# Kernel tuning notes

Hardware: AMD Instinct MI355X
Metric: run time of the kernel (lower is better)

The kernel has to match this reference:

```python
import jax, jax.numpy as jnp
import numpy as np

N_NODES = 50000
N_EDGES = 1600000
N_GRAPHS = 64


def _gcn_conv(x, row, col, ew, W, b, n_nodes):
    # x: [N, Fin] -> [N, Fout]; PyG GCNConv: lin, add self-loops (w=1),
    # symmetric normalization, scatter-add at target (col), + bias.
    x = x @ W
    loop = jnp.arange(n_nodes, dtype=row.dtype)
    r = jnp.concatenate([row, loop])
    c = jnp.concatenate([col, loop])
    w = jnp.concatenate([ew, jnp.ones((n_nodes,), dtype=ew.dtype)])
    deg = jax.ops.segment_sum(w, c, num_segments=n_nodes)
    dinv = jnp.where(deg > 0, jax.lax.rsqrt(jnp.where(deg > 0, deg, 1.0)), 0.0)
    norm = dinv[r] * w * dinv[c]                      # [E+N]
    msg = x[r] * norm[:, None]                        # [E+N, Fout] (dominant traffic)
    out = jax.ops.segment_sum(msg, c, num_segments=n_nodes)
    return out + b


def setup_inputs() -> dict:
    key = jax.random.key(0)
    ks = jax.random.split(key, 12)
    x = jax.random.normal(ks[0], (N_NODES, 128), dtype=jnp.float32)
    edge_index = jax.random.randint(ks[1], (2, N_EDGES), 0, N_NODES, dtype=jnp.int32)
    edge_attr = jax.random.uniform(ks[2], (N_EDGES,), dtype=jnp.float32)
    batch = jnp.sort(jax.random.randint(ks[3], (N_NODES,), 0, N_GRAPHS, dtype=jnp.int32))
    glorot = lambda k, fi, fo: jax.random.normal(k, (fi, fo), jnp.float32) * np.sqrt(2.0 / (fi + fo))
    return {
        "x": x, "edge_index": edge_index, "edge_attr": edge_attr, "batch": batch,
        "W1": glorot(ks[4], 128, 128), "b1": jnp.zeros((128,), jnp.float32),
        "W2": glorot(ks[5], 128, 64), "b2": jnp.zeros((64,), jnp.float32),
        "fc1_W": glorot(ks[6], 64, 128), "fc1_b": jnp.zeros((128,), jnp.float32),
        "fc2_W": glorot(ks[7], 128, 2), "fc2_b": jnp.zeros((2,), jnp.float32),
    }


def reference(x, edge_index, edge_attr, batch, W1, b1, W2, b2, fc1_W, fc1_b, fc2_W, fc2_b):
    row, col = edge_index[0], edge_index[1]
    h = jax.nn.relu(_gcn_conv(x, row, col, edge_attr, W1, b1, N_NODES))
    x1 = jax.nn.relu(_gcn_conv(h, row, col, edge_attr, W2, b2, N_NODES))
    # global mean pool over batch ids
    sums = jax.ops.segment_sum(x1, batch, num_segments=N_GRAPHS)
    cnt = jax.ops.segment_sum(jnp.ones((N_NODES,), x1.dtype), batch, num_segments=N_GRAPHS)
    x2 = sums / jnp.maximum(cnt, 1.0)[:, None]        # [B, 64]
    # dropout is identity in eval mode
    h = jax.nn.relu(x2 @ fc1_W + fc1_b)
    logits = h @ fc2_W + fc2_b                        # [B, 2]
    return jax.nn.log_softmax(logits, axis=1)
```

## Files before the change

kernel.cpp:

```cpp
#include <hip/hip_runtime.h>
#include <hip/hip_bf16.h>


#define CAP 64
#define OVFCAP 8192
#define NRANGE 512
#define MAXNRP 2048
#define BSTR 68
#define KP 136
#define PARTNB 256
#define PBUF 6400

typedef float v2f  __attribute__((ext_vector_type(2)));
typedef float f32x4 __attribute__((ext_vector_type(4)));
typedef short bf16x8 __attribute__((ext_vector_type(8)));

__device__ inline unsigned short f2bf(float f) {
    unsigned u = __float_as_uint(f);
    u += 0x7FFFu + ((u >> 16) & 1u);
    return (unsigned short)(u >> 16);
}
__device__ inline void fp8x4_to_f32(unsigned w, float* o) {
    v2f lo = __builtin_amdgcn_cvt_pk_f32_fp8((int)w, false);
    v2f hi = __builtin_amdgcn_cvt_pk_f32_fp8((int)w, true);
    o[0] = lo[0]; o[1] = lo[1]; o[2] = hi[0]; o[3] = hi[1];
}
__device__ inline unsigned f32x4_to_fp8(float a, float b, float c, float d) {
    int w = 0;
    w = __builtin_amdgcn_cvt_pk_fp8_f32(a, b, w, false);
    w = __builtin_amdgcn_cvt_pk_fp8_f32(c, d, w, true);
    return (unsigned)w;
}
__device__ inline float dinv_of(int ws) {
    return rsqrtf((float)ws * (1.0f / 32768.0f) + 1.0f);
}

__global__ __launch_bounds__(512)
void part_kernel(const int* __restrict__ rows, const int* __restrict__ cols,
                 const float* __restrict__ ew, int* __restrict__ rangeCnt,
                 uint2* __restrict__ rng, int E, int NR, int RSEG,
                 const float* __restrict__ W1, const float* __restrict__ W2,
                 unsigned short* __restrict__ wt1, unsigned short* __restrict__ wt2) {
    const int t = threadIdx.x;
    if (blockIdx.x >= PARTNB) {
        if (blockIdx.x == PARTNB) {
            for (int i = t; i < 128 * 128; i += 512) {
                int c = i >> 7, k = i & 127;
                wt1[c * KP + k] = f2bf(W1[k * 128 + c]);
            }
        } else {
            for (int i = t; i < 64 * 128; i += 512) {
                int c = i >> 7, k = i & 127;
                wt2[c * KP + k] = f2bf(W2[k * 64 + c]);
            }
        }
        return;
    }
    __shared__ uint2 buf[PBUF];
    __shared__ int hcnt[NRANGE];
    __shared__ int lbase[NRANGE];
    __shared__ int gbase[NRANGE];
    __shared__ int wtot[8];
    const int CS = (E + PARTNB - 1) / PARTNB;
    const int e0 = blockIdx.x * CS, e1 = min(e0 + CS, E);
    const int M = e1 - e0;

    if (CS <= PBUF) {
        for (int i = t; i < NRANGE; i += 512) hcnt[i] = 0;
        __syncthreads();
        for (int e = e0 + t; e < e1; e += 512)
            atomicAdd(&hcnt[cols[e] / NR], 1);
        __syncthreads();
        {
            int v = hcnt[t];
            int inc = v;
            #pragma unroll
            for (int off = 1; off < 64; off <<= 1) {
                int n = __shfl_up(inc, off);
                if ((t & 63) >= off) inc += n;
            }
            const int w = t >> 6;
            if ((t & 63) == 63) wtot[w] = inc;
            __syncthreads();
            int wo = 0;
            for (int k = 0; k < w; ++k) wo += wtot[k];
            int excl = wo + inc - v;
            lbase[t] = excl;
            gbase[t] = (v > 0) ? atomicAdd(&rangeCnt[t], v) : 0;
            hcnt[t] = excl;
        }
        __syncthreads();
        for (int e = e0 + t; e < e1; e += 512) {
            int c = cols[e];
            int r = c / NR;
            int q = (int)(ew[e] * 32768.0f);
            if (q > 32767) q = 32767;
            unsigned rec = ((unsigned)rows[e] << 15) | (unsigned)q;
            int p = atomicAdd(&hcnt[r], 1);
            buf[p] = make_uint2((unsigned)c, rec);
        }
        __syncthreads();
        for (int i = t; i < M; i += 512) {
            uint2 u = buf[i];
            int r = (int)u.x / NR;
            int idx = gbase[r] + (i - lbase[r]);
            if (idx < RSEG) rng[(size_t)r * RSEG + idx] = u;
        }
    } else {
        for (int i = t; i < NRANGE; i += 512) hcnt[i] = 0;
        __syncthreads();
        for (int e = e0 + t; e < e1; e += 512)
            atomicAdd(&hcnt[cols[e] / NR], 1);
        __syncthreads();
        for (int i = t; i < NRANGE; i += 512)
            hcnt[i] = atomicAdd(&rangeCnt[i], hcnt[i]);
        __syncthreads();
        for (int e = e0 + t; e < e1; e += 512) {
            int c = cols[e];
            int r = c / NR;
            int q = (int)(ew[e] * 32768.0f);
            if (q > 32767) q = 32767;
            unsigned rec = ((unsigned)rows[e] << 15) | (unsigned)q;
            int pos = atomicAdd(&hcnt[r], 1);
            if (pos < RSEG) rng[(size_t)r * RSEG + pos] = make_uint2((unsigned)c, rec);
        }
    }
}

__global__ __launch_bounds__(512)
void place_kernel(const uint2* __restrict__ rng, const int* __restrict__ rangeCnt,
                  int* __restrict__ cnt, int* __restrict__ wsum,
                  unsigned* __restrict__ slot, int4* __restrict__ ovf,
                  int* __restrict__ ovfcnt, int NR, int RSEG, int N) {
    __shared__ int cur[MAXNRP];
    __shared__ int wsl[MAXNRP];
    const int r = blockIdx.x;
    const int t = threadIdx.x;
    const int n0 = r * NR;
    for (int n = t; n < NR; n += 512) { cur[n] = 0; wsl[n] = 0; }
    __syncthreads();
    const int M = min(rangeCnt[r], RSEG);
    const uint2* lst = rng + (size_t)r * RSEG;
    for (int k = t; k < M; k += 512) {
        uint2 u2 = lst[k];
        int cl = (int)u2.x - n0;
        int q = (int)(u2.y & 32767u);
        int pos = atomicAdd(&cur[cl], 1);
        atomicAdd(&wsl[cl], q);
        if (pos < CAP) {
            slot[(size_t)u2.x * CAP + pos] = u2.y;
        } else {
            int o = atomicAdd(ovfcnt, 1);
            if (o < OVFCAP)
                ovf[o] = make_int4((int)(u2.y >> 15), (int)u2.x, q, 0);
        }
    }
    __syncthreads();
    for (int n = t; n < NR; n += 512) {
        int gn = n0 + n;
        if (gn < N) { cnt[gn] = cur[n]; wsum[gn] = wsl[n]; }
    }
}

__global__ void place_simple_kernel(const int* __restrict__ rows, const int* __restrict__ cols,
                                    const float* __restrict__ ew, int* __restrict__ cnt,
                                    int* __restrict__ wsum,
                                    unsigned* __restrict__ slot, int4* __restrict__ ovf,
                                    int* __restrict__ ovfcnt, int E) {
    int e = blockIdx.x * 256 + threadIdx.x;
    if (e >= E) return;
    int r = rows[e], c = cols[e];
    int q = (int)(ew[e] * 32768.0f);
    if (q > 32767) q = 32767;
    int pos = atomicAdd(&cnt[c], 1);
    atomicAdd(&wsum[c], q);
    if (pos < CAP) {
        slot[(size_t)c * CAP + pos] = ((unsigned)r << 15) | (unsigned)q;
    } else {
        int o = atomicAdd(ovfcnt, 1);
        if (o < OVFCAP) ovf[o] = make_int4(r, c, q, 0);
    }
}

template <int BN, bool AF32>
__global__ __launch_bounds__(256)
void gemm_mfma_kernel(const void* __restrict__ Av, const unsigned short* __restrict__ wt,
                      const int* __restrict__ wsum, unsigned char* __restrict__ outf8,
                      int M) {
    constexpr int CT = BN / 16;
    constexpr int EPS = BN + 4;
    __shared__ unsigned short wl[BN * KP];
    __shared__ float ep[4][16 * EPS];
    const int t = threadIdx.x;
    for (int i = t; i < BN * KP / 8; i += 256)
        ((uint4*)wl)[i] = ((const uint4*)wt)[i];
    __syncthreads();
    const int w = t >> 6, lane = t & 63;
    const int n16 = lane & 15, q = lane >> 4;
    const int rowBase = blockIdx.x * 64 + w * 16;
    int arow = rowBase + n16; if (arow >= M) arow = M - 1;
    f32x4 acc[CT];
    #pragma unroll
    for (int ct = 0; ct < CT; ++ct) acc[ct] = (f32x4){0.f, 0.f, 0.f, 0.f};
    #pragma unroll
    for (int kt = 0; kt < 4; ++kt) {
        bf16x8 af;
        if (AF32) {
            const float* ap = (const float*)Av + (size_t)arow * 128 + kt * 32 + q * 8;
            float4 a0 = *(const float4*)ap;
            float4 a1 = *(const float4*)(ap + 4);
            af[0] = (short)f2bf(a0.x); af[1] = (short)f2bf(a0.y);
            af[2] = (short)f2bf(a0.z); af[3] = (short)f2bf(a0.w);
            af[4] = (short)f2bf(a1.x); af[5] = (short)f2bf(a1.y);
            af[6] = (short)f2bf(a1.z); af[7] = (short)f2bf(a1.w);
        } else {
            af = *(const bf16x8*)((const unsigned short*)Av + (size_t)arow * 128 + kt * 32 + q * 8);
        }
        #pragma unroll
        for (int ct = 0; ct < CT; ++ct) {
            bf16x8 bfr = *(const bf16x8*)&wl[(ct * 16 + n16) * KP + kt * 32 + q * 8];
            acc[ct] = __builtin_amdgcn_mfma_f32_16x16x32_bf16(af, bfr, acc[ct], 0, 0, 0);
        }
    }
    #pragma unroll
    for (int ct = 0; ct < CT; ++ct)
        #pragma unroll
        for (int r = 0; r < 4; ++r)
            ep[w][(q * 4 + r) * EPS + ct * 16 + n16] = acc[ct][r];
    __syncthreads();
    const int lr = lane & 15;
    const int cc = (lane >> 4) * (BN / 4);
    int grow = rowBase + lr;
    if (grow < M) {
        float s = dinv_of(wsum[grow]);
        const float* src = &ep[w][lr * EPS + cc];
        #pragma unroll
        for (int u = 0; u < BN / 64; ++u) {
            int col0 = cc + u * 16;
            int slice = col0 >> 6, cw = col0 & 63;
            unsigned w0 = f32x4_to_fp8(src[u*16+ 0]*s, src[u*16+ 1]*s, src[u*16+ 2]*s, src[u*16+ 3]*s);
            unsigned w1 = f32x4_to_fp8(src[u*16+ 4]*s, src[u*16+ 5]*s, src[u*16+ 6]*s, src[u*16+ 7]*s);
            unsigned w2 = f32x4_to_fp8(src[u*16+ 8]*s, src[u*16+ 9]*s, src[u*16+10]*s, src[u*16+11]*s);
            unsigned w3 = f32x4_to_fp8(src[u*16+12]*s, src[u*16+13]*s, src[u*16+14]*s, src[u*16+15]*s);
            *(uint4*)&outf8[((size_t)slice * M + grow) * 64 + cw] = make_uint4(w0, w1, w2, w3);
        }
    }
}

template <int F, int S, bool OB, bool POOL>
__global__ void gather_kernel(const unsigned char* __restrict__ xsb,
                              const unsigned* __restrict__ slot,
                              const int* __restrict__ cnt, const int* __restrict__ wsum,
                              const float* __restrict__ b, const int4* __restrict__ ovf,
                              const int* __restrict__ ovfcnt, void* __restrict__ outv, int N,
                              const int* __restrict__ gbatch, float* __restrict__ gsums,
                              float* __restrict__ gcnt) {
    constexpr int EPN = 4;
    __shared__ unsigned sbkt[16 * BSTR];
    __shared__ float x1s[16 * 68];
    __shared__ int gidl[16];
    const int slice = (S > 1) ? ((int)blockIdx.x % S) : 0;
    const int grp = (S > 1) ? ((int)blockIdx.x / S) : blockIdx.x;
    const int t = threadIdx.x;
    const int node0 = grp * 16;
    {
        int ndl = t >> 4, part = t & 15;
        int snode = node0 + ndl; if (snode >= N) snode = N - 1;
        int sc = cnt[snode]; if (sc > CAP) sc = CAP;
        if (part * 4 < sc)
            *(uint4*)&sbkt[ndl * BSTR + part * 4] =
                *(const uint4*)&slot[(size_t)snode * CAP + part * 4];
    }
    if constexpr (POOL) {
        if (t < 16) {
            int sn = node0 + t;
            gidl[t] = (sn < N) ? gbatch[sn] : -1;
        }
    }
    __syncthreads();
    const int w = t >> 6, lane = t & 63;
    const int cg = lane & 3;
    const int e  = (lane >> 2) & 3;
    const int nd = lane >> 4;
    const int ndl = w * 4 + nd;
    const int i = node0 + ndl;
    const bool iv = (i < N);
    const int ic = iv ? i : 0;
    const uint4* xs4 = (const uint4*)(xsb + (size_t)slice * N * 64);
    int mraw = iv ? cnt[ic] : 0;
    int m = mraw > CAP ? CAP : mraw;
    const unsigned* lb = &sbkt[ndl * BSTR];
    float acc[16] = {};
    int j = e;
    for (; j + EPN < m; j += 2 * EPN) {
        unsigned u0 = lb[j], u1 = lb[j + EPN];
        float c0 = (float)(u0 & 32767u), c1 = (float)(u1 & 32767u);
        uint4 a0 = xs4[(size_t)(u0 >> 15) * 4 + cg];
        uint4 a1 = xs4[(size_t)(u1 >> 15) * 4 + cg];
        float f0[16], f1[16];
        fp8x4_to_f32(a0.x, f0 + 0);  fp8x4_to_f32(a0.y, f0 + 4);
        fp8x4_to_f32(a0.z, f0 + 8);  fp8x4_to_f32(a0.w, f0 + 12);
        fp8x4_to_f32(a1.x, f1 + 0);  fp8x4_to_f32(a1.y, f1 + 4);
        fp8x4_to_f32(a1.z, f1 + 8);  fp8x4_to_f32(a1.w, f1 + 12);
        #pragma unroll
        for (int k = 0; k < 16; ++k) acc[k] += f0[k] * c0 + f1[k] * c1;
    }
    if (j < m) {
        unsigned u = lb[j];
        float c = (float)(u & 32767u);
        uint4 a = xs4[(size_t)(u >> 15) * 4 + cg];
        float f[16];
        fp8x4_to_f32(a.x, f + 0);  fp8x4_to_f32(a.y, f + 4);
        fp8x4_to_f32(a.z, f + 8);  fp8x4_to_f32(a.w, f + 12);
        #pragma unroll
        for (int k = 0; k < 16; ++k) acc[k] += f[k] * c;
    }
    if (mraw > CAP) {
        int oc = *ovfcnt; if (oc > OVFCAP) oc = OVFCAP;
        for (int k = e; k < oc; k += EPN) {
            int4 r4 = ovf[k];
            if (r4.y == i) {
                float c = (float)r4.z;
                uint4 a = xs4[(size_t)r4.x * 4 + cg];
                float f[16];
                fp8x4_to_f32(a.x, f + 0);  fp8x4_to_f32(a.y, f + 4);
                fp8x4_to_f32(a.z, f + 8);  fp8x4_to_f32(a.w, f + 12);
                #pragma unroll
                for (int kk = 0; kk < 16; ++kk) acc[kk] += f[kk] * c;
            }
        }
    }
    #pragma unroll
    for (int k = 0; k < 16; ++k) {
        acc[k] += __shfl_xor(acc[k], 4);
        acc[k] += __shfl_xor(acc[k], 8);
    }
    if (e == 0 && iv) {
        float d = dinv_of(wsum[i]);
        float sa = d * (1.0f / 32768.0f);
        uint4 sv = xs4[(size_t)i * 4 + cg];
        float sf[16];
        fp8x4_to_f32(sv.x, sf + 0);  fp8x4_to_f32(sv.y, sf + 4);
        fp8x4_to_f32(sv.z, sf + 8);  fp8x4_to_f32(sv.w, sf + 12);
        const float* bb = &b[slice * 64 + cg * 16];
        float o[16];
        #pragma unroll
        for (int k = 0; k < 16; ++k)
            o[k] = fmaxf(acc[k] * sa + sf[k] * d + bb[k], 0.f);
        if (OB) {
            unsigned short* dst = (unsigned short*)outv + (size_t)i * F + slice * 64 + cg * 16;
            unsigned pw[8];
            #pragma unroll
            for (int k = 0; k < 8; ++k)
                pw[k] = (unsigned)f2bf(o[2 * k]) | ((unsigned)f2bf(o[2 * k + 1]) << 16);
            *(uint4*)&dst[0] = make_uint4(pw[0], pw[1], pw[2], pw[3]);
            *(uint4*)&dst[8] = make_uint4(pw[4], pw[5], pw[6], pw[7]);
        } else if constexpr (!POOL) {
            float* dst = (float*)outv + (size_t)i * F + slice * 64 + cg * 16;
            *(float4*)&dst[0]  = make_float4(o[0], o[1], o[2], o[3]);
            *(float4*)&dst[4]  = make_float4(o[4], o[5], o[6], o[7]);
            *(float4*)&dst[8]  = make_float4(o[8], o[9], o[10], o[11]);
            *(float4*)&dst[12] = make_float4(o[12], o[13], o[14], o[15]);
        } else {
            float* dst = &x1s[ndl * 68 + cg * 16];
            *(float4*)&dst[0]  = make_float4(o[0], o[1], o[2], o[3]);
            *(float4*)&dst[4]  = make_float4(o[4], o[5], o[6], o[7]);
            *(float4*)&dst[8]  = make_float4(o[8], o[9], o[10], o[11]);
            *(float4*)&dst[12] = make_float4(o[12], o[13], o[14], o[15]);
        }
    }
    if constexpr (POOL) {
        __syncthreads();
        if (t < 64) {
            const int f = t;
            float run = 0.f; int gcur = -1;
            #pragma unroll 4
            for (int n = 0; n < 16; ++n) {
                int g = gidl[n];
                if (g < 0) break;
                if (g != gcur) {
                    if (gcur >= 0) atomicAdd(&gsums[gcur * 64 + f], run);
                    run = 0.f; gcur = g;
                }
                run += x1s[n * 68 + f];
            }
            if (gcur >= 0) atomicAdd(&gsums[gcur * 64 + f], run);
        } else if (t == 64) {
            float rc = 0.f; int gcur = -1;
            for (int n = 0; n < 16; ++n) {
                int g = gidl[n];
                if (g < 0) break;
                if (g != gcur) {
                    if (gcur >= 0) atomicAdd(&gcnt[gcur], rc);
                    rc = 0.f; gcur = g;
                }
                rc += 1.f;
            }
            if (gcur >= 0) atomicAdd(&gcnt[gcur], rc);
        }
    }
}

__global__ void head_kernel(const float* __restrict__ sums, const float* __restrict__ cnt,
                            const float* __restrict__ fc1W, const float* __restrict__ fc1b,
                            const float* __restrict__ fc2W, const float* __restrict__ fc2b,
                            float* __restrict__ out) {
    __shared__ float x2s[64];
    __shared__ float hs[128];
    __shared__ float lg[2];
    const int g = blockIdx.x;
    const int t = threadIdx.x;
    if (t < 64) {
        float c = fmaxf(cnt[g], 1.f);
        x2s[t] = sums[g * 64 + t] / c;
    }
    __syncthreads();
    {
        float a = fc1b[t];
        #pragma unroll 8
        for (int j = 0; j < 64; ++j) a += x2s[j] * fc1W[j * 128 + t];
        hs[t] = fmaxf(a, 0.f);
    }
    __syncthreads();
    {
        int m = t >> 6, l = t & 63;
        float p = hs[l] * fc2W[l * 2 + m] + hs[l + 64] * fc2W[(l + 64) * 2 + m];
        #pragma unroll
        for (int off = 1; off < 64; off <<= 1) p += __shfl_xor(p, off);
        if (l == 0) lg[m] = p + fc2b[m];
    }
    __syncthreads();
    if (t == 0) {
        float l0 = lg[0], l1 = lg[1];
        float mx = fmaxf(l0, l1);
        float lse = mx + logf(expf(l0 - mx) + expf(l1 - mx));
        out[g * 2 + 0] = l0 - lse;
        out[g * 2 + 1] = l1 - lse;
    }
}

extern "C" void kernel_launch(void* const* d_in, const int* in_sizes, int n_in,
                              void* d_out, int out_size, void* d_ws, size_t ws_size,
                              hipStream_t stream) {
    const float* x      = (const float*)d_in[0];
    const int*   eidx   = (const int*)d_in[1];
    const float* ew     = (const float*)d_in[2];
    const int*   batch  = (const int*)d_in[3];
    const float* W1     = (const float*)d_in[4];
    const float* b1     = (const float*)d_in[5];
    const float* W2     = (const float*)d_in[6];
    const float* b2     = (const float*)d_in[7];
    const float* fc1W   = (const float*)d_in[8];
    const float* fc1b   = (const float*)d_in[9];
    const float* fc2W   = (const float*)d_in[10];
    const float* fc2b   = (const float*)d_in[11];
    float* out = (float*)d_out;

    const int N = in_sizes[3];
    const int E = in_sizes[2];
    const int G = 64;
    const int* rows = eidx;
    const int* cols = eidx + E;
    const int NR = (N + NRANGE - 1) / NRANGE;
    const int RSEG = E / NRANGE + 2048;

    float* ws = (float*)d_ws;
    size_t off = 0;
    auto alloc = [&](size_t n) { float* p = ws + off; off += (n + 15) & ~(size_t)15; return p; };
    float*    sums     = alloc(64 * 64);
    float*    cntf     = alloc(16);
    int*      ovfcnt   = (int*)alloc(16);
    int*      rangeCnt = (int*)alloc(NRANGE);
    int*      cnt      = (int*)alloc(N);
    int*      wsum     = (int*)alloc(N);
    size_t zfloats = off;
    unsigned short* wt1 = (unsigned short*)alloc(128 * KP / 2 + 16);
    unsigned short* wt2 = (unsigned short*)alloc(64 * KP / 2 + 16);
    unsigned* slot   = (unsigned*)alloc((size_t)N * CAP);
    int4*     ovf    = (int4*)alloc((size_t)OVFCAP * 4);
    float*    bufA   = alloc((size_t)N * 128);
    float*    bufB   = alloc((size_t)N * 128);
    unsigned char*  xw1f8 = (unsigned char*)bufA;
    unsigned char*  xw2f8 = (unsigned char*)bufA;
    uint2*          rng   = (uint2*)bufB;
    unsigned short* hbf   = (unsigned short*)bufB;
    (void)ws_size;

    hipMemsetAsync(d_ws, 0, zfloats * sizeof(float), stream);

    const bool fits = (NR <= MAXNRP) &&
                      ((size_t)NRANGE * RSEG * sizeof(uint2) <= (size_t)N * 512);
    if (fits) {
        part_kernel<<<PARTNB + 2, 512, 0, stream>>>(rows, cols, ew, rangeCnt, rng, E, NR, RSEG,
                                                    W1, W2, wt1, wt2);
        place_kernel<<<NRANGE, 512, 0, stream>>>(rng, rangeCnt, cnt, wsum, slot, ovf, ovfcnt,
                                                 NR, RSEG, N);
    } else {
        part_kernel<<<PARTNB + 2, 512, 0, stream>>>(rows, cols, ew, rangeCnt, rng, 0, NR, RSEG,
                                                    W1, W2, wt1, wt2);
        place_simple_kernel<<<(E + 255) / 256, 256, 0, stream>>>(rows, cols, ew, cnt, wsum,
                                                                 slot, ovf, ovfcnt, E);
    }

    gemm_mfma_kernel<128, true><<<(N + 63) / 64, 256, 0, stream>>>(x, wt1, wsum, xw1f8, N);
    gather_kernel<128, 2, true, false><<<((N + 15) / 16) * 2, 256, 0, stream>>>(
        xw1f8, slot, cnt, wsum, b1, ovf, ovfcnt, hbf, N, nullptr, nullptr, nullptr);

    gemm_mfma_kernel<64, false><<<(N + 63) / 64, 256, 0, stream>>>(hbf, wt2, wsum, xw2f8, N);
    gather_kernel<64, 1, false, true><<<(N + 15) / 16, 256, 0, stream>>>(
        xw2f8, slot, cnt, wsum, b2, ovf, ovfcnt, nullptr, N, batch, sums, cntf);

    head_kernel<<<G, 128, 0, stream>>>(sums, cntf, fc1W, fc1b, fc2W, fc2b, out);
}
```

Measured before the change: 213.9 us.

## Fuse layer-1 gather with layer-2 GEMM in one kernel

```diff
diff --git a/kernel.cpp b/kernel.cpp
--- a/kernel.cpp
+++ b/kernel.cpp
@@ -243,6 +243,141 @@
             unsigned w2 = f32x4_to_fp8(src[u*16+ 8]*s, src[u*16+ 9]*s, src[u*16+10]*s, src[u*16+11]*s);
             unsigned w3 = f32x4_to_fp8(src[u*16+12]*s, src[u*16+13]*s, src[u*16+14]*s, src[u*16+15]*s);
             *(uint4*)&outf8[((size_t)slice * M + grow) * 64 + cw] = make_uint4(w0, w1, w2, w3);
+        }
+    }
+}
+
+__global__ __launch_bounds__(512)
+void g1g2_kernel(const unsigned char* __restrict__ xsb,
+                 const unsigned* __restrict__ slot,
+                 const int* __restrict__ cnt, const int* __restrict__ wsum,
+                 const float* __restrict__ b1, const unsigned short* __restrict__ wt2,
+                 const int4* __restrict__ ovf, const int* __restrict__ ovfcnt,
+                 unsigned char* __restrict__ xw2f8, int N) {
+    constexpr int EPN = 4;
+    __shared__ unsigned sbkt[16 * BSTR];
+    __shared__ unsigned short hs[16 * KP];
+    __shared__ unsigned short wl[64 * KP];
+    __shared__ float ep[16 * 68];
+    const int t = threadIdx.x;
+    const int node0 = blockIdx.x * 16;
+    for (int i = t; i < 64 * KP / 8; i += 512)
+        ((uint4*)wl)[i] = ((const uint4*)wt2)[i];
+    for (int i = t; i < 16 * KP / 8; i += 512)
+        ((uint4*)hs)[i] = make_uint4(0, 0, 0, 0);
+    if (t < 256) {
+        int ndl = t >> 4, part = t & 15;
+        int snode = node0 + ndl; if (snode >= N) snode = N - 1;
+        int sc = cnt[snode]; if (sc > CAP) sc = CAP;
+        if (part * 4 < sc)
+            *(uint4*)&sbkt[ndl * BSTR + part * 4] =
+                *(const uint4*)&slot[(size_t)snode * CAP + part * 4];
+    }
+    __syncthreads();
+    const int cg  = t & 7;
+    const int e   = (t >> 3) & 3;
+    const int ndl = t >> 5;
+    const int i = node0 + ndl;
+    const bool iv = (i < N);
+    const int ic = iv ? i : 0;
+    const int cg3 = cg & 3;
+    const size_t sb = (size_t)(cg >> 2) * N;
+    const uint4* xs4 = (const uint4*)xsb;
+    int mraw = iv ? cnt[ic] : 0;
+    int m = mraw > CAP ? CAP : mraw;
+    const unsigned* lb = &sbkt[ndl * BSTR];
+    float acc[16] = {};
+    int j = e;
+    for (; j + EPN < m; j += 2 * EPN) {
+        unsigned u0 = lb[j], u1 = lb[j + EPN];
+        float c0 = (float)(u0 & 32767u), c1 = (float)(u1 & 32767u);
+        uint4 a0 = xs4[(sb + (u0 >> 15)) * 4 + cg3];
+        uint4 a1 = xs4[(sb + (u1 >> 15)) * 4 + cg3];
+        float f0[16], f1[16];
+        fp8x4_to_f32(a0.x, f0 + 0);  fp8x4_to_f32(a0.y, f0 + 4);
+        fp8x4_to_f32(a0.z, f0 + 8);  fp8x4_to_f32(a0.w, f0 + 12);
+        fp8x4_to_f32(a1.x, f1 + 0);  fp8x4_to_f32(a1.y, f1 + 4);
+        fp8x4_to_f32(a1.z, f1 + 8);  fp8x4_to_f32(a1.w, f1 + 12);
+        #pragma unroll
+        for (int k = 0; k < 16; ++k) acc[k] += f0[k] * c0 + f1[k] * c1;
+    }
+    if (j < m) {
+        unsigned u = lb[j];
+        float c = (float)(u & 32767u);
+        uint4 a = xs4[(sb + (u >> 15)) * 4 + cg3];
+        float f[16];
+        fp8x4_to_f32(a.x, f + 0);  fp8x4_to_f32(a.y, f + 4);
+        fp8x4_to_f32(a.z, f + 8);  fp8x4_to_f32(a.w, f + 12);
+        #pragma unroll
+        for (int k = 0; k < 16; ++k) acc[k] += f[k] * c;
+    }
+    if (mraw > CAP) {
+        int oc = *ovfcnt; if (oc > OVFCAP) oc = OVFCAP;
+        for (int k = e; k < oc; k += EPN) {
+            int4 r4 = ovf[k];
+            if (r4.y == i) {
+                float c = (float)r4.z;
+                uint4 a = xs4[(sb + r4.x) * 4 + cg3];
+                float f[16];
+                fp8x4_to_f32(a.x, f + 0);  fp8x4_to_f32(a.y, f + 4);
+                fp8x4_to_f32(a.z, f + 8);  fp8x4_to_f32(a.w, f + 12);
+                #pragma unroll
+                for (int kk = 0; kk < 16; ++kk) acc[kk] += f[kk] * c;
+            }
+        }
+    }
+    #pragma unroll
+    for (int k = 0; k < 16; ++k) {
+        acc[k] += __shfl_xor(acc[k], 8);
+        acc[k] += __shfl_xor(acc[k], 16);
+    }
+    if (e == 0 && iv) {
+        float d = dinv_of(wsum[i]);
+        float sa = d * (1.0f / 32768.0f);
+        uint4 sv = xs4[(sb + i) * 4 + cg3];
+        float sf[16];
+        fp8x4_to_f32(sv.x, sf + 0);  fp8x4_to_f32(sv.y, sf + 4);
+        fp8x4_to_f32(sv.z, sf + 8);  fp8x4_to_f32(sv.w, sf + 12);
+        const float* bb = &b1[cg * 16];
+        float o[16];
+        #pragma unroll
+        for (int k = 0; k < 16; ++k)
+            o[k] = fmaxf(acc[k] * sa + sf[k] * d + bb[k], 0.f);
+        unsigned short* dst = &hs[ndl * KP + cg * 16];
+        unsigned pw[8];
+        #pragma unroll
+        for (int k = 0; k < 8; ++k)
+            pw[k] = (unsigned)f2bf(o[2 * k]) | ((unsigned)f2bf(o[2 * k + 1]) << 16);
+        *(uint4*)&dst[0] = make_uint4(pw[0], pw[1], pw[2], pw[3]);
+        *(uint4*)&dst[8] = make_uint4(pw[4], pw[5], pw[6], pw[7]);
+    }
+    __syncthreads();
+    const int w = t >> 6, lane = t & 63;
+    if (w < 4) {
+        const int n16 = lane & 15, q = lane >> 4;
+        f32x4 a2 = (f32x4){0.f, 0.f, 0.f, 0.f};
+        #pragma unroll
+        for (int kt = 0; kt < 4; ++kt) {
+            bf16x8 af = *(const bf16x8*)&hs[(lane & 15) * KP + kt * 32 + q * 8];
+            bf16x8 bfr = *(const bf16x8*)&wl[(w * 16 + n16) * KP + kt * 32 + q * 8];
+            a2 = __builtin_amdgcn_mfma_f32_16x16x32_bf16(af, bfr, a2, 0, 0, 0);
+        }
+        #pragma unroll
+        for (int r = 0; r < 4; ++r)
+            ep[(q * 4 + r) * 68 + w * 16 + n16] = a2[r];
+    }
+    __syncthreads();
+    if (t < 64) {
+        int lr = t & 15, chunk = t >> 4;
+        int grow = node0 + lr;
+        if (grow < N) {
+            float s = dinv_of(wsum[grow]);
+            const float* src = &ep[lr * 68 + chunk * 16];
+            unsigned w0 = f32x4_to_fp8(src[ 0]*s, src[ 1]*s, src[ 2]*s, src[ 3]*s);
+            unsigned w1 = f32x4_to_fp8(src[ 4]*s, src[ 5]*s, src[ 6]*s, src[ 7]*s);
+            unsigned w2 = f32x4_to_fp8(src[ 8]*s, src[ 9]*s, src[10]*s, src[11]*s);
+            unsigned w3 = f32x4_to_fp8(src[12]*s, src[13]*s, src[14]*s, src[15]*s);
+            *(uint4*)&xw2f8[(size_t)grow * 64 + chunk * 16] = make_uint4(w0, w1, w2, w3);
         }
     }
 }
@@ -481,9 +616,8 @@
     float*    bufA   = alloc((size_t)N * 128);
     float*    bufB   = alloc((size_t)N * 128);
     unsigned char*  xw1f8 = (unsigned char*)bufA;
-    unsigned char*  xw2f8 = (unsigned char*)bufA;
+    unsigned char*  xw2f8 = (unsigned char*)bufA + (size_t)2 * N * 64;
     uint2*          rng   = (uint2*)bufB;
-    unsigned short* hbf   = (unsigned short*)bufB;
     (void)ws_size;
 
     hipMemsetAsync(d_ws, 0, zfloats * sizeof(float), stream);
@@ -503,10 +637,10 @@
     }
 
     gemm_mfma_kernel<128, true><<<(N + 63) / 64, 256, 0, stream>>>(x, wt1, wsum, xw1f8, N);
-    gather_kernel<128, 2, true, false><<<((N + 15) / 16) * 2, 256, 0, stream>>>(
-        xw1f8, slot, cnt, wsum, b1, ovf, ovfcnt, hbf, N, nullptr, nullptr, nullptr);
-
-    gemm_mfma_kernel<64, false><<<(N + 63) / 64, 256, 0, stream>>>(hbf, wt2, wsum, xw2f8, N);
+
+    g1g2_kernel<<<(N + 15) / 16, 512, 0, stream>>>(xw1f8, slot, cnt, wsum, b1, wt2,
+                                                   ovf, ovfcnt, xw2f8, N);
+
     gather_kernel<64, 1, false, true><<<(N + 15) / 16, 256, 0, stream>>>(
         xw2f8, slot, cnt, wsum, b2, ovf, ovfcnt, nullptr, N, batch, sums, cntf);
 
```

Result: no change. 216.8 us (+1.3%).
